# Optimization experiments

Measured on AMD Instinct MI355X. Metric: run time of the kernel, lower is better.

## Reference

```python
import jax, jax.numpy as jnp
import numpy as np

# ---- module hyperparameters (from init_kwargs) ----
N_REPL = 4      # n
NUM_FM = 32
D = 2
PRD = 2
K_SZ = 2 * D + 1
ALPHA = 0.1
ETA = 0.1
THETA = 0.1
EPS = 1e-10


def symm_pad(x, p):
    # faithful to torch symm_pad: sequential in-place border reflection
    x = x.at[..., :p, :].set(jnp.flip(x[..., p:2 * p, :], axis=-2))
    x = x.at[..., -p:, :].set(jnp.flip(x[..., -2 * p:-p, :], axis=-2))
    x = x.at[..., :, :p].set(jnp.flip(x[..., :, p:2 * p], axis=-1))
    x = x.at[..., :, -p:].set(jnp.flip(x[..., :, -2 * p:-p], axis=-1))
    return x


def pad_activations(A, prd=PRD, d=D):
    H, W = A.shape[-2], A.shape[-1]
    pz = jnp.zeros(A.shape[:-2] + (prd * d + H, prd * d + W), A.dtype)
    pz = pz.at[..., prd:-prd, prd:-prd].set(A)
    return symm_pad(pz, 2 * prd)


def minmax_on_fm(x):
    # min-max normalize each feature map (last two dims) to [0,1]
    mn = x.min(axis=(-2, -1), keepdims=True)
    mx = x.max(axis=(-2, -1), keepdims=True)
    return (x - mn) / (mx - mn + EPS)


def softmax_on_fm(x):
    sh = x.shape
    return jax.nn.softmax(x.reshape(sh[:-2] + (-1,)), axis=-1).reshape(sh)


def softmax_minmax_scaled(x):
    return softmax_on_fm(minmax_on_fm(x))


def conv2d(x, w):
    # x: (B, Cin, H, W), w: (Cout, Cin, k, k), valid conv
    return jax.lax.conv_general_dilated(
        x, w, window_strides=(1, 1), padding='VALID',
        dimension_numbers=('NCHW', 'OIHW', 'NCHW'))


def setup_inputs() -> dict:
    key = jax.random.key(0)
    kA, kK, kN = jax.random.split(key, 3)
    C = N_REPL * NUM_FM
    A = jax.random.uniform(kA, (16, NUM_FM, 56, 56), jnp.float32)
    # K initialized as softmax_on_fm(rand), matching __init__
    K = softmax_on_fm(jax.random.uniform(kK, (C, C, K_SZ, K_SZ), jnp.float32))
    noise = jax.random.normal(kN, (16, C, 56, 56), jnp.float32)
    return {"A": A, "K": K, "noise": noise}


def reference(A, K, noise):
    B, num_fm, H, W = A.shape
    n, d, prd, k = N_REPL, D, PRD, K_SZ
    C = n * num_fm

    A = symm_pad(A, prd)                              # (B, num_fm, H, W)
    Ab = jnp.tile(A, (1, n, 1, 1))                    # (B, C, H, W)
    Ab = jnp.clip(Ab + ETA * noise, 0.0)
    pA = pad_activations(Ab)                          # (B, C, H+4, W+4)

    # torch does K.transpose_(0,1) in place; K1 is the post-transpose K
    K1 = jnp.swapaxes(K, 0, 1)
    L = conv2d(pA, minmax_on_fm(K1)) / num_fm         # (B, C, H, W)
    L = softmax_minmax_scaled(L)

    # winner-take-all across the n replicas of each feature map
    s = (Ab + L).sum(axis=(-2, -1)).reshape(B, n, num_fm)
    winners = jnp.argmax(jnp.swapaxes(s, 1, 2), axis=-1)          # (B, num_fm)
    fm_idx = num_fm * winners + jnp.arange(num_fm)                # (B, num_fm)
    win_mask = jnp.zeros((B, C), Ab.dtype).at[
        jnp.arange(B)[:, None], fm_idx].set(1.0)                  # 1 at winning channels

    # ---- Hebbian K update: per-offset masked cross-correlation ----
    Am = Ab * win_mask[:, :, None, None]  # zero losing *source* channels
    cols = []
    for x in range(k):
        xo = -d + x
        rows = []
        for y in range(k):
            yo = -d + y
            src = Am[:, :, max(0, xo):H + min(xo, 0), max(0, yo):W + min(yo, 0)]
            tgt = Ab[:, :, max(0, -xo):H + min(-xo, 0), max(0, -yo):W + min(-yo, 0)]
            rows.append(jnp.einsum('bchw,bahw->ca', src, tgt) / (C * B))
        cols.append(jnp.stack(rows, axis=-1))        # (C, C, k) over y
    K_change = jnp.stack(cols, axis=-2)              # (C, C, k, k) indexed [c,a,x,y]

    K2 = (1.0 - ALPHA) * K1 + ALPHA * minmax_on_fm(K_change)

    # ---- second lateral pass with losing channels zeroed ----
    A2 = Ab * win_mask[:, :, None, None]
    # torch zeroes only diagonal filters K[c,c] of losing c per sample; since the
    # corresponding input channels of A2 are exactly zero, a single shared-weight
    # conv is mathematically identical.
    L2 = conv2d(pad_activations(A2), minmax_on_fm(jnp.swapaxes(K2, 0, 1))) / num_fm

    gather = lambda X: jnp.take_along_axis(X, fm_idx[:, :, None, None], axis=1)
    O = gather(A2) + THETA * gather(L2)              # (B, num_fm, H, W)
    return O
```

## Files before the change

kernel.cpp:

```cpp
#include <hip/hip_runtime.h>


typedef __attribute__((ext_vector_type(8))) short short8;
typedef __attribute__((ext_vector_type(4))) float floatx4;

#define EPSF 1e-10f

__device__ __forceinline__ int map60(int r) {
  return r < 4 ? 5 - r : (r < 56 ? r - 2 : 109 - r);
}
__device__ __forceinline__ unsigned short f2bf(float x) {
  unsigned int u = __float_as_uint(x);
  u += 0x7fff + ((u >> 16) & 1);
  return (unsigned short)(u >> 16);
}
__device__ __forceinline__ float bf2f(unsigned int h) {
  return __uint_as_float((h & 0xffffu) << 16);
}

__global__ __launch_bounds__(256) void k1_build(const float* __restrict__ A,
                                                const float* __restrict__ noise,
                                                unsigned short* __restrict__ Abf,
                                                float* __restrict__ s) {
  int bc = blockIdx.x;
  int b = bc >> 7, c = bc & 127;
  int fm = c & 31;
  const float* Abase = A + (size_t)(b * 32 + fm) * 3136;
  const float* nz = noise + (size_t)bc * 3136;
  unsigned short* outb = Abf + 128 + (size_t)bc * 3840;
  float local = 0.f;
  for (int idx = threadIdx.x; idx < 3840; idx += 256) {
    int r = idx >> 6, col = idx & 63;
    int h = r - 2, w = col - 2;
    float v = 0.f;
    if ((unsigned)h < 56u && (unsigned)w < 56u) {
      int hh = h < 2 ? 3 - h : (h >= 54 ? 107 - h : h);
      int ww = w < 2 ? 3 - w : (w >= 54 ? 107 - w : w);
      v = fmaxf(Abase[hh * 56 + ww] + 0.1f * nz[h * 56 + w], 0.f);
      local += v;
    }
    outb[idx] = f2bf(v);
  }
  int lane = threadIdx.x & 63, wid = threadIdx.x >> 6;
  float v = local;
  for (int off = 32; off; off >>= 1) v += __shfl_down(v, off, 64);
  __shared__ float red[4];
  if (lane == 0) red[wid] = v;
  __syncthreads();
  if (threadIdx.x == 0) s[bc] = red[0] + red[1] + red[2] + red[3];
}

__global__ __launch_bounds__(512) void k2_winners(const float* __restrict__ s,
                                                  int* __restrict__ fm_idx,
                                                  int* __restrict__ cmask,
                                                  unsigned short* __restrict__ Abf) {
  int t = threadIdx.x;
  {
    int b = t >> 5, f = t & 31;
    float best = s[b * 128 + f];
    int bn = 0;
    for (int n = 1; n < 4; n++) {
      float v = s[b * 128 + n * 32 + f];
      if (v > best) { best = v; bn = n; }
    }
    fm_idx[t] = bn * 32 + f;
  }
  if (t < 128) Abf[t] = 0;
  if (t >= 384) Abf[128 + 7864320 + (t - 384)] = 0;
  __syncthreads();
  if (t < 128) {
    int m = 0;
    for (int b = 0; b < 16; b++)
      if (fm_idx[b * 32 + (t & 31)] == t) m |= (1 << b);
    cmask[t] = m;
  }
}

__global__ __launch_bounds__(256) void k2c_shift(const unsigned short* __restrict__ Abf,
                                                 const int* __restrict__ fm_idx,
                                                 unsigned short* __restrict__ Sb) {
  int bx = blockIdx.x;
  int g = bx & 31, di = (bx >> 5) % 5, b = bx / 160;
  int dy = di - 2;
  int c = fm_idx[b * 32 + g];
  const unsigned short* src = Abf + 128 + (size_t)(b * 128 + c) * 3840;
  unsigned short* dst = Sb + (size_t)(b * 5 + di) * 122880 + g * 3840;
  for (int q = threadIdx.x; q < 960; q += 256) {
    int p0 = q * 4;
    unsigned short h[4];
#pragma unroll
    for (int j = 0; j < 4; j++) {
      int sp = p0 + j - dy;
      h[j] = ((unsigned)sp < 3840u) ? src[sp] : (unsigned short)0;
    }
    uint2 w;
    w.x = h[0] | ((unsigned)h[1] << 16);
    w.y = h[2] | ((unsigned)h[3] << 16);
    *reinterpret_cast<uint2*>(dst + p0) = w;
  }
}

__global__ __launch_bounds__(256) void k2t_transpose(const unsigned short* __restrict__ Abf,
                                                     const int* __restrict__ fm_idx,
                                                     unsigned short* __restrict__ T) {
  __shared__ int win[32];
  int b = blockIdx.x / 15, chunk = blockIdx.x % 15;
  if (threadIdx.x < 32) win[threadIdx.x] = fm_idx[b * 32 + threadIdx.x];
  __syncthreads();
  int p = chunk * 256 + threadIdx.x;
  int r = p >> 6, s2 = p & 63;
  int mr = map60(r) + 2;
  int ms = (s2 < 60) ? map60(s2) + 2 : -1;
  unsigned int out[16];
#pragma unroll
  for (int gp = 0; gp < 16; gp++) {
    unsigned short v0 = 0, v1 = 0;
    if (ms >= 0) {
      v0 = Abf[128 + ((size_t)(b * 128) + win[2 * gp]) * 3840 + mr * 64 + ms];
      v1 = Abf[128 + ((size_t)(b * 128) + win[2 * gp + 1]) * 3840 + mr * 64 + ms];
    }
    out[gp] = (unsigned)v0 | ((unsigned)v1 << 16);
  }
  uint4* dst = reinterpret_cast<uint4*>(T + (size_t)b * 122880 + (size_t)p * 32);
#pragma unroll
  for (int q = 0; q < 4; q++) {
    uint4 u;
    u.x = out[4 * q]; u.y = out[4 * q + 1]; u.z = out[4 * q + 2]; u.w = out[4 * q + 3];
    dst[q] = u;
  }
}

__global__ __launch_bounds__(256, 1) void k3_mfma(const unsigned short* __restrict__ Sb,
                                                  const unsigned short* __restrict__ Abf,
                                                  float* __restrict__ Kc_b) {
  int bx = blockIdx.x;
  int nt = bx & 7, mt = (bx >> 3) & 1, b = bx >> 4;
  int wave = threadIdx.x >> 6, lane = threadIdx.x & 63;
  int al = lane & 15, quad = lane >> 4;
  int g0 = mt * 16, a0 = nt * 16;
  int k0 = wave * 960;
  floatx4 acc[5][5];
#pragma unroll
  for (int i = 0; i < 5; i++)
#pragma unroll
    for (int j = 0; j < 5; j++) acc[i][j] = (floatx4){0.f, 0.f, 0.f, 0.f};
  const short8* pA[5];
#pragma unroll
  for (int di = 0; di < 5; di++)
    pA[di] = reinterpret_cast<const short8*>(
        Sb + (size_t)(b * 5 + di) * 122880 + (size_t)(g0 + al) * 3840 + k0 + quad * 8);
  const short8* pB = reinterpret_cast<const short8*>(
      Abf + 128 + (size_t)(b * 128 + a0 + al) * 3840 + k0 + quad * 8) - 16;
  for (int ks = 0; ks < 30; ks++) {
    short8 afr[5], bfr[5];
#pragma unroll
    for (int d = 0; d < 5; d++) afr[d] = pA[d][0];
#pragma unroll
    for (int d = 0; d < 5; d++) bfr[d] = pB[d * 8];
#pragma unroll
    for (int di = 0; di < 5; di++)
#pragma unroll
      for (int dj = 0; dj < 5; dj++)
        acc[di][dj] =
            __builtin_amdgcn_mfma_f32_16x16x32_bf16(afr[di], bfr[dj], acc[di][dj], 0, 0, 0);
#pragma unroll
    for (int d = 0; d < 5; d++) pA[d] += 4;
    pB += 4;
  }
  __shared__ float red[6400];
  float* myrow = red + lane * 100;
  if (wave == 0) {
#pragma unroll
    for (int di = 0; di < 5; di++)
#pragma unroll
      for (int dj = 0; dj < 5; dj++)
#pragma unroll
        for (int r = 0; r < 4; r++) myrow[(di * 5 + dj) * 4 + r] = acc[di][dj][r];
  }
  __syncthreads();
#pragma unroll
  for (int w = 1; w < 4; w++) {
    if (wave == w) {
#pragma unroll
      for (int di = 0; di < 5; di++)
#pragma unroll
        for (int dj = 0; dj < 5; dj++)
#pragma unroll
          for (int r = 0; r < 4; r++) myrow[(di * 5 + dj) * 4 + r] += acc[di][dj][r];
    }
    __syncthreads();
  }
  if (wave == 0) {
#pragma unroll
    for (int di = 0; di < 5; di++)
#pragma unroll
      for (int dj = 0; dj < 5; dj++) {
        int t_out = 24 - (dj * 5 + di);
#pragma unroll
        for (int r = 0; r < 4; r++) {
          int g = g0 + quad * 4 + r;
          Kc_b[(((size_t)b * 32 + g) * 128 + (a0 + al)) * 25 + t_out] =
              myrow[(di * 5 + dj) * 4 + r] * (1.0f / 2048.0f);
        }
      }
  }
}

__global__ __launch_bounds__(256) void k4_weights(const float* __restrict__ Kc_b,
                                                  const float* __restrict__ K,
                                                  const int* __restrict__ cmask,
                                                  float* __restrict__ W2) {
  int gid = blockIdx.x * 256 + threadIdx.x;
  int o = gid >> 7, i = gid & 127;
  int m = cmask[i];
  float kc[25];
#pragma unroll
  for (int t = 0; t < 25; t++) kc[t] = 0.f;
  for (int b = 0; b < 16; b++) {
    if ((m >> b) & 1) {
      const float* p = Kc_b + (((size_t)b * 32 + (i & 31)) * 128 + o) * 25;
#pragma unroll
      for (int t = 0; t < 25; t++) kc[t] += p[t];
    }
  }
  float mn = 1e30f, mx = -1e30f;
#pragma unroll
  for (int t = 0; t < 25; t++) { mn = fminf(mn, kc[t]); mx = fmaxf(mx, kc[t]); }
  float d1 = mx - mn + EPSF;
  const float* kp = K + ((size_t)o * 128 + i) * 25;
  float k2[25], mn2 = 1e30f, mx2 = -1e30f;
#pragma unroll
  for (int t = 0; t < 25; t++) {
    k2[t] = 0.9f * kp[t] + 0.1f * ((kc[t] - mn) / d1);
    mn2 = fminf(mn2, k2[t]);
    mx2 = fmaxf(mx2, k2[t]);
  }
  float d2 = mx2 - mn2 + EPSF;
#pragma unroll
  for (int t = 0; t < 25; t++) W2[(size_t)gid * 25 + t] = (k2[t] - mn2) / d2;
}

__global__ __launch_bounds__(256) void k4b_gather(const float* __restrict__ W2,
                                                  const int* __restrict__ fm_idx,
                                                  unsigned short* __restrict__ W2g) {
  int tid = blockIdx.x * 256 + threadIdx.x;
  int b = tid >> 10, f = (tid >> 5) & 31, g = tid & 31;
  int o = fm_idx[b * 32 + f], i = fm_idx[b * 32 + g];
  const float* src = W2 + ((size_t)o * 128 + i) * 25;
#pragma unroll
  for (int t = 0; t < 25; t++)
    W2g[((size_t)((b * 25 + t) * 32 + f) << 5) + g] = f2bf(src[t]);
}

__global__ __launch_bounds__(64) void k5_mfma(const unsigned short* __restrict__ W2g,
                                              const unsigned short* __restrict__ T,
                                              const unsigned short* __restrict__ Abf,
                                              const int* __restrict__ fm_idx,
                                              float* __restrict__ O) {
  int bx = blockIdx.x;
  int rg = bx % 14;
  int mtb = bx / 14;
  int mt = mtb & 1, b = mtb >> 1;
  int lane = threadIdx.x, al = lane & 15, quad = lane >> 4;
  int fm = mt * 16 + al;
  short8 afr[25];
#pragma unroll
  for (int t = 0; t < 25; t++)
    afr[t] = *reinterpret_cast<const short8*>(
        W2g + ((size_t)((b * 25 + t) * 32 + fm) << 5) + quad * 8);
  int orow[4];
#pragma unroll
  for (int r = 0; r < 4; r++) orow[r] = fm_idx[b * 32 + mt * 16 + quad * 4 + r];
  const unsigned short* Tb = T + (size_t)b * 122880;
  for (int rr = 0; rr < 4; rr++) {
    int row = 2 + rg * 4 + rr;
    for (int pair = 0; pair < 2; pair++) {
      int px0 = row * 64 + pair * 32 + al;
      floatx4 acca = (floatx4){0.f, 0.f, 0.f, 0.f};
      floatx4 accb = (floatx4){0.f, 0.f, 0.f, 0.f};
#pragma unroll
      for (int t = 0; t < 25; t++) {
        int off = (t / 5 - 2) * 64 + (t % 5) - 2;
        const short8* pb = reinterpret_cast<const short8*>(
            Tb + (ptrdiff_t)(px0 + off) * 32 + quad * 8);
        short8 b0 = pb[0];
        short8 b1 = pb[64];
        acca = __builtin_amdgcn_mfma_f32_16x16x32_bf16(afr[t], b0, acca, 0, 0, 0);
        accb = __builtin_amdgcn_mfma_f32_16x16x32_bf16(afr[t], b1, accb, 0, 0, 0);
      }
      int h = row - 2;
#pragma unroll
      for (int half = 0; half < 2; half++) {
        floatx4 acc = half ? accb : acca;
        int cc = pair * 32 + half * 16 + al;
        if (cc >= 2 && cc < 58) {
          int w = cc - 2;
          int px = row * 64 + cc;
#pragma unroll
          for (int r = 0; r < 4; r++) {
            int f = mt * 16 + quad * 4 + r;
            float base = bf2f(Abf[128 + (size_t)(b * 128 + orow[r]) * 3840 + px]);
            O[(size_t)(b * 32 + f) * 3136 + h * 56 + w] = base + acc[r] * (0.1f / 32.0f);
          }
        }
      }
    }
  }
}

extern "C" void kernel_launch(void* const* d_in, const int* in_sizes, int n_in,
                              void* d_out, int out_size, void* d_ws, size_t ws_size,
                              hipStream_t stream) {
  const float* A = (const float*)d_in[0];
  const float* K = (const float*)d_in[1];
  const float* noise = (const float*)d_in[2];
  float* O = (float*)d_out;

  float* ws = (float*)d_ws;
  unsigned short* Abf = (unsigned short*)ws;
  float* s = ws + 3932288;
  int* fm_idx = (int*)(ws + 3934336);
  int* cmask = (int*)(ws + 3934848);
  float* Kc_b = ws + 3934976;
  unsigned short* T = (unsigned short*)(ws + 5573376);
  unsigned short* Sb = (unsigned short*)(ws + 6556416);
  float* W2 = ws + 6556416;
  unsigned short* W2g = (unsigned short*)(ws + 6966016);

  k1_build<<<2048, 256, 0, stream>>>(A, noise, Abf, s);
  k2_winners<<<1, 512, 0, stream>>>(s, fm_idx, cmask, Abf);
  k2c_shift<<<2560, 256, 0, stream>>>(Abf, fm_idx, Sb);
  k2t_transpose<<<240, 256, 0, stream>>>(Abf, fm_idx, T);
  k3_mfma<<<256, 256, 0, stream>>>(Sb, Abf, Kc_b);
  k4_weights<<<64, 256, 0, stream>>>(Kc_b, K, cmask, W2);
  k4b_gather<<<64, 256, 0, stream>>>(W2, fm_idx, W2g);
  k5_mfma<<<448, 64, 0, stream>>>(W2g, T, Abf, fm_idx, O);
}
```

Before: 182.1 us.

## Vectorize build and shift kernels, split K in MFMA, fuse weight gather

The build kernel now loads and stores four elements per thread, with a fast interior path using float2 loads and packed bf16 stores. The shift kernel makes all five shifted copies from one 16-byte load using alignbit, so it needs five times fewer blocks. The correlation MFMA kernel splits the reduction dimension in two to double the block count, writing per-half partials that the weight kernel sums. The weight kernel writes the bf16 gathered weights directly for each winning sample, which removes the separate gather kernel and the fp32 W2 buffer, at the cost of more scattered stores and a larger partial buffer.

```diff
diff --git a/kernel.cpp b/kernel.cpp
--- a/kernel.cpp
+++ b/kernel.cpp
@@ -29,17 +29,44 @@
   const float* nz = noise + (size_t)bc * 3136;
   unsigned short* outb = Abf + 128 + (size_t)bc * 3840;
   float local = 0.f;
-  for (int idx = threadIdx.x; idx < 3840; idx += 256) {
-    int r = idx >> 6, col = idx & 63;
-    int h = r - 2, w = col - 2;
-    float v = 0.f;
-    if ((unsigned)h < 56u && (unsigned)w < 56u) {
+  for (int q = threadIdx.x; q < 960; q += 256) {
+    int r = q >> 4, qc = q & 15, col0 = qc << 2;
+    int h = r - 2;
+    float v0, v1, v2, v3;
+    if (r < 2 || r > 57 || qc == 15) {
+      v0 = v1 = v2 = v3 = 0.f;
+    } else if (r >= 4 && r <= 55 && qc >= 1 && qc <= 13) {
+      int w0 = col0 - 2;
+      const float* ap = Abase + h * 56 + w0;
+      const float* np = nz + h * 56 + w0;
+      float2 a0 = *reinterpret_cast<const float2*>(ap);
+      float2 a1 = *reinterpret_cast<const float2*>(ap + 2);
+      float2 n0 = *reinterpret_cast<const float2*>(np);
+      float2 n1 = *reinterpret_cast<const float2*>(np + 2);
+      v0 = fmaxf(a0.x + 0.1f * n0.x, 0.f);
+      v1 = fmaxf(a0.y + 0.1f * n0.y, 0.f);
+      v2 = fmaxf(a1.x + 0.1f * n1.x, 0.f);
+      v3 = fmaxf(a1.y + 0.1f * n1.y, 0.f);
+    } else {
+      float vv[4];
       int hh = h < 2 ? 3 - h : (h >= 54 ? 107 - h : h);
-      int ww = w < 2 ? 3 - w : (w >= 54 ? 107 - w : w);
-      v = fmaxf(Abase[hh * 56 + ww] + 0.1f * nz[h * 56 + w], 0.f);
-      local += v;
-    }
-    outb[idx] = f2bf(v);
+#pragma unroll
+      for (int j = 0; j < 4; j++) {
+        int w = col0 + j - 2;
+        float v = 0.f;
+        if ((unsigned)w < 56u) {
+          int ww = w < 2 ? 3 - w : (w >= 54 ? 107 - w : w);
+          v = fmaxf(Abase[hh * 56 + ww] + 0.1f * nz[h * 56 + w], 0.f);
+        }
+        vv[j] = v;
+      }
+      v0 = vv[0]; v1 = vv[1]; v2 = vv[2]; v3 = vv[3];
+    }
+    local += v0 + v1 + v2 + v3;
+    uint2 w;
+    w.x = (unsigned)f2bf(v0) | ((unsigned)f2bf(v1) << 16);
+    w.y = (unsigned)f2bf(v2) | ((unsigned)f2bf(v3) << 16);
+    *reinterpret_cast<uint2*>(outb + r * 64 + col0) = w;
   }
   int lane = threadIdx.x & 63, wid = threadIdx.x >> 6;
   float v = local;
@@ -80,23 +107,33 @@
                                                  const int* __restrict__ fm_idx,
                                                  unsigned short* __restrict__ Sb) {
   int bx = blockIdx.x;
-  int g = bx & 31, di = (bx >> 5) % 5, b = bx / 160;
-  int dy = di - 2;
+  int g = bx & 31, b = bx >> 5;
   int c = fm_idx[b * 32 + g];
   const unsigned short* src = Abf + 128 + (size_t)(b * 128 + c) * 3840;
-  unsigned short* dst = Sb + (size_t)(b * 5 + di) * 122880 + g * 3840;
-  for (int q = threadIdx.x; q < 960; q += 256) {
-    int p0 = q * 4;
-    unsigned short h[4];
-#pragma unroll
-    for (int j = 0; j < 4; j++) {
-      int sp = p0 + j - dy;
-      h[j] = ((unsigned)sp < 3840u) ? src[sp] : (unsigned short)0;
-    }
-    uint2 w;
-    w.x = h[0] | ((unsigned)h[1] << 16);
-    w.y = h[2] | ((unsigned)h[3] << 16);
-    *reinterpret_cast<uint2*>(dst + p0) = w;
+  unsigned short* dbase = Sb + (size_t)b * 5 * 122880 + g * 3840;
+  for (int q = threadIdx.x; q < 480; q += 256) {
+    int p0 = q * 8;
+    uint4 M = *reinterpret_cast<const uint4*>(src + p0);
+    unsigned L = (q == 0) ? 0u : *reinterpret_cast<const unsigned*>(src + p0 - 2);
+    unsigned R = (q == 479) ? 0u : *reinterpret_cast<const unsigned*>(src + p0 + 8);
+    unsigned u0 = L, u1 = M.x, u2 = M.y, u3 = M.z, u4 = M.w, u5 = R;
+    uint4 o;
+    o.x = u0; o.y = u1; o.z = u2; o.w = u3;
+    *reinterpret_cast<uint4*>(dbase + 4 * 122880 + p0) = o;
+    o.x = __builtin_amdgcn_alignbit(u1, u0, 16);
+    o.y = __builtin_amdgcn_alignbit(u2, u1, 16);
+    o.z = __builtin_amdgcn_alignbit(u3, u2, 16);
+    o.w = __builtin_amdgcn_alignbit(u4, u3, 16);
+    *reinterpret_cast<uint4*>(dbase + 3 * 122880 + p0) = o;
+    o.x = u1; o.y = u2; o.z = u3; o.w = u4;
+    *reinterpret_cast<uint4*>(dbase + 2 * 122880 + p0) = o;
+    o.x = __builtin_amdgcn_alignbit(u2, u1, 16);
+    o.y = __builtin_amdgcn_alignbit(u3, u2, 16);
+    o.z = __builtin_amdgcn_alignbit(u4, u3, 16);
+    o.w = __builtin_amdgcn_alignbit(u5, u4, 16);
+    *reinterpret_cast<uint4*>(dbase + 1 * 122880 + p0) = o;
+    o.x = u2; o.y = u3; o.z = u4; o.w = u5;
+    *reinterpret_cast<uint4*>(dbase + p0) = o;
   }
 }
 
@@ -130,15 +167,15 @@
   }
 }
 
-__global__ __launch_bounds__(256, 1) void k3_mfma(const unsigned short* __restrict__ Sb,
-                                                  const unsigned short* __restrict__ Abf,
-                                                  float* __restrict__ Kc_b) {
+__global__ __launch_bounds__(256) void k3_mfma(const unsigned short* __restrict__ Sb,
+                                               const unsigned short* __restrict__ Abf,
+                                               float* __restrict__ Kc_b) {
   int bx = blockIdx.x;
-  int nt = bx & 7, mt = (bx >> 3) & 1, b = bx >> 4;
+  int nt = bx & 7, mt = (bx >> 3) & 1, kh = (bx >> 4) & 1, b = bx >> 5;
   int wave = threadIdx.x >> 6, lane = threadIdx.x & 63;
   int al = lane & 15, quad = lane >> 4;
   int g0 = mt * 16, a0 = nt * 16;
-  int k0 = wave * 960;
+  int k0 = kh * 1920 + wave * 480;
   floatx4 acc[5][5];
 #pragma unroll
   for (int i = 0; i < 5; i++)
@@ -151,7 +188,7 @@
         Sb + (size_t)(b * 5 + di) * 122880 + (size_t)(g0 + al) * 3840 + k0 + quad * 8);
   const short8* pB = reinterpret_cast<const short8*>(
       Abf + 128 + (size_t)(b * 128 + a0 + al) * 3840 + k0 + quad * 8) - 16;
-  for (int ks = 0; ks < 30; ks++) {
+  for (int ks = 0; ks < 15; ks++) {
     short8 afr[5], bfr[5];
 #pragma unroll
     for (int d = 0; d < 5; d++) afr[d] = pA[d][0];
@@ -191,6 +228,7 @@
     __syncthreads();
   }
   if (wave == 0) {
+    int slot = b * 2 + kh;
 #pragma unroll
     for (int di = 0; di < 5; di++)
 #pragma unroll
@@ -199,7 +237,7 @@
 #pragma unroll
         for (int r = 0; r < 4; r++) {
           int g = g0 + quad * 4 + r;
-          Kc_b[(((size_t)b * 32 + g) * 128 + (a0 + al)) * 25 + t_out] =
+          Kc_b[(((size_t)slot * 32 + g) * 128 + (a0 + al)) * 25 + t_out] =
               myrow[(di * 5 + dj) * 4 + r] * (1.0f / 2048.0f);
         }
       }
@@ -209,16 +247,16 @@
 __global__ __launch_bounds__(256) void k4_weights(const float* __restrict__ Kc_b,
                                                   const float* __restrict__ K,
                                                   const int* __restrict__ cmask,
-                                                  float* __restrict__ W2) {
+                                                  unsigned short* __restrict__ W2g) {
   int gid = blockIdx.x * 256 + threadIdx.x;
   int o = gid >> 7, i = gid & 127;
-  int m = cmask[i];
+  int mi = cmask[i], mo = cmask[o];
   float kc[25];
 #pragma unroll
   for (int t = 0; t < 25; t++) kc[t] = 0.f;
-  for (int b = 0; b < 16; b++) {
-    if ((m >> b) & 1) {
-      const float* p = Kc_b + (((size_t)b * 32 + (i & 31)) * 128 + o) * 25;
+  for (int slot = 0; slot < 32; slot++) {
+    if ((mi >> (slot >> 1)) & 1) {
+      const float* p = Kc_b + (((size_t)slot * 32 + (i & 31)) * 128 + o) * 25;
 #pragma unroll
       for (int t = 0; t < 25; t++) kc[t] += p[t];
     }
@@ -236,20 +274,18 @@
     mx2 = fmaxf(mx2, k2[t]);
   }
   float d2 = mx2 - mn2 + EPSF;
-#pragma unroll
-  for (int t = 0; t < 25; t++) W2[(size_t)gid * 25 + t] = (k2[t] - mn2) / d2;
-}
-
-__global__ __launch_bounds__(256) void k4b_gather(const float* __restrict__ W2,
-                                                  const int* __restrict__ fm_idx,
-                                                  unsigned short* __restrict__ W2g) {
-  int tid = blockIdx.x * 256 + threadIdx.x;
-  int b = tid >> 10, f = (tid >> 5) & 31, g = tid & 31;
-  int o = fm_idx[b * 32 + f], i = fm_idx[b * 32 + g];
-  const float* src = W2 + ((size_t)o * 128 + i) * 25;
-#pragma unroll
-  for (int t = 0; t < 25; t++)
-    W2g[((size_t)((b * 25 + t) * 32 + f) << 5) + g] = f2bf(src[t]);
+  unsigned short wb[25];
+#pragma unroll
+  for (int t = 0; t < 25; t++) wb[t] = f2bf((k2[t] - mn2) / d2);
+  int mw = mo & mi;
+  int f = o & 31, g = i & 31;
+  while (mw) {
+    int b = __ffs(mw) - 1;
+    mw &= mw - 1;
+    unsigned short* dst = W2g + ((size_t)(b * 25) * 32 + f) * 32 + g;
+#pragma unroll
+    for (int t = 0; t < 25; t++) dst[(size_t)t * 1024] = wb[t];
+  }
 }
 
 __global__ __launch_bounds__(64) void k5_mfma(const unsigned short* __restrict__ W2g,
@@ -322,17 +358,15 @@
   int* fm_idx = (int*)(ws + 3934336);
   int* cmask = (int*)(ws + 3934848);
   float* Kc_b = ws + 3934976;
-  unsigned short* T = (unsigned short*)(ws + 5573376);
-  unsigned short* Sb = (unsigned short*)(ws + 6556416);
-  float* W2 = ws + 6556416;
-  unsigned short* W2g = (unsigned short*)(ws + 6966016);
+  unsigned short* T = (unsigned short*)(ws + 7211776);
+  unsigned short* Sb = (unsigned short*)(ws + 8194816);
+  unsigned short* W2g = (unsigned short*)(ws + 8194816);
 
   k1_build<<<2048, 256, 0, stream>>>(A, noise, Abf, s);
   k2_winners<<<1, 512, 0, stream>>>(s, fm_idx, cmask, Abf);
-  k2c_shift<<<2560, 256, 0, stream>>>(Abf, fm_idx, Sb);
+  k2c_shift<<<512, 256, 0, stream>>>(Abf, fm_idx, Sb);
   k2t_transpose<<<240, 256, 0, stream>>>(Abf, fm_idx, T);
-  k3_mfma<<<256, 256, 0, stream>>>(Sb, Abf, Kc_b);
-  k4_weights<<<64, 256, 0, stream>>>(Kc_b, K, cmask, W2);
-  k4b_gather<<<64, 256, 0, stream>>>(W2, fm_idx, W2g);
+  k3_mfma<<<512, 256, 0, stream>>>(Sb, Abf, Kc_b);
+  k4_weights<<<64, 256, 0, stream>>>(Kc_b, K, cmask, W2g);
   k5_mfma<<<448, 64, 0, stream>>>(W2g, T, Abf, fm_idx, O);
 }
```

Measured after the change: 188.3 us. 3.4% more time.
